# Kernel optimization log

Hardware: AMD Instinct MI355X
Metric: run time of the kernel (lower is better)

The kernel has to match this reference:

```python
import jax, jax.numpy as jnp
import numpy as np

SCORE_THRESH = 0.5
NMS_THRESH = 0.4
TOP_K = 1000  # fixed pre-NMS candidate budget (jit-safe replacement for boolean masking)
STRIDES = (8, 16, 32)
H, W = 2176, 3840


def _anchor_centers(fh, fw, stride):
    yv, xv = jnp.meshgrid(jnp.arange(fh), jnp.arange(fw), indexing='ij')
    return (jnp.stack([xv, yv], -1).reshape(-1, 2).astype(jnp.float32)) * stride  # [N,2]


def _decode_level(scores, bbox, kps, stride):
    fh, fw = H // stride, W // stride
    c = _anchor_centers(fh, fw, stride)                 # [N,2]
    s = jax.nn.sigmoid(scores.reshape(-1))              # [N]
    d = bbox.reshape(-1, 4) * stride                    # [N,4]
    boxes = jnp.concatenate([c - d[:, :2], c + d[:, 2:4]], axis=1)  # x1y1x2y2
    k = kps.reshape(-1, 5, 2) * stride + c[:, None, :]  # (x,y) pairs
    return s, boxes, k.reshape(-1, 10)


def _iou_matrix(b):
    area = (b[:, 2] - b[:, 0]) * (b[:, 3] - b[:, 1])
    lt = jnp.maximum(b[:, None, :2], b[None, :, :2])
    rb = jnp.minimum(b[:, None, 2:], b[None, :, 2:])
    wh = jnp.clip(rb - lt, 0.0)
    inter = wh[..., 0] * wh[..., 1]
    return inter / jnp.clip(area[:, None] + area[None, :] - inter, 1e-9)


def _nms_keep(iou, valid):
    n = iou.shape[0]
    ar = jnp.arange(n)

    def body(i, keep):
        sup = (iou[i] > NMS_THRESH) & (ar > i) & keep[i]
        return keep & ~sup

    return jax.lax.fori_loop(0, n, body, valid)


def reference(x, scores8, bbox8, kps8, scores16, bbox16, kps16, scores32, bbox32, kps32):
    levels = ((scores8, bbox8, kps8), (scores16, bbox16, kps16), (scores32, bbox32, kps32))
    ss, bs, ks = [], [], []
    for (s, b, k), stride in zip(levels, STRIDES):
        si, bi, ki = _decode_level(s, b, k, stride)
        ss.append(si); bs.append(bi); ks.append(ki)
    scores = jnp.concatenate(ss)   # [N_total]
    boxes = jnp.concatenate(bs)    # [N_total,4]
    kpss = jnp.concatenate(ks)     # [N_total,10]

    masked = jnp.where(scores > SCORE_THRESH, scores, -1.0)
    top_s, idx = jax.lax.top_k(masked, TOP_K)
    valid = top_s > SCORE_THRESH
    b = boxes[idx]
    k = kpss[idx]

    keep = jax.lax.stop_gradient(_nms_keep(_iou_matrix(b), valid))
    final_boxes = jnp.where(keep[:, None], b, 0.0)
    final_scores = jnp.where(keep, top_s, 0.0)
    final_kpss = jnp.where(keep[:, None], k, 0.0)
    return final_boxes, final_scores, final_kpss


def setup_inputs() -> dict:
    key = jax.random.key(0)
    ks = jax.random.split(key, 10)
    n8 = (H // 8) * (W // 8)
    n16 = (H // 16) * (W // 16)
    n32 = (H // 32) * (W // 32)
    return {
        'x': jax.random.normal(ks[0], (1, 3, H, W), jnp.float32),
        'scores8': jax.random.normal(ks[1], (1, n8, 1), jnp.float32),
        'bbox8': jax.random.uniform(ks[2], (1, n8, 4), jnp.float32),
        'kps8': jax.random.normal(ks[3], (1, n8, 10), jnp.float32),
        'scores16': jax.random.normal(ks[4], (1, n16, 1), jnp.float32),
        'bbox16': jax.random.uniform(ks[5], (1, n16, 4), jnp.float32),
        'kps16': jax.random.normal(ks[6], (1, n16, 10), jnp.float32),
        'scores32': jax.random.normal(ks[7], (1, n32, 1), jnp.float32),
        'bbox32': jax.random.uniform(ks[8], (1, n32, 4), jnp.float32),
        'kps32': jax.random.normal(ks[9], (1, n32, 10), jnp.float32),
    }
```

## Files before the change

kernel.cpp:

```cpp
#include <hip/hip_runtime.h>
#include <stdint.h>

typedef unsigned int u32;
typedef unsigned long long u64;

#define N8   130560
#define N16  32640
#define N32  8160
#define NTOT 171360
#define NTOT4 42840
#define TOPK 1000
#define NWORDS 16
#define NBINS 4096
#define BUCKET_SCALE 682.0f
#define LIST_CAP 2016
#define CPB 32
#define HIST_BLKS 168
#define RED_BLKS 32
#define RANK_BLKS 63
#define IOU_BLKS 63
#define IOU_TASKS (TOPK * NWORDS)
#define NMS_CACHE 256


#define MI_B   0
#define MI_CNT 1
#define META_U32 256

#define OFF_PART 0
#define OFF_RED  1376256
#define OFF_META 1392640
#define OFF_NZ   1393664
#define OFF_LIST 1393792
#define OFF_MASK 1409920

__device__ __forceinline__ u32 bucket_of(float x) {
  u32 b = (u32)(x * BUCKET_SCALE);
  return b > (NBINS - 1) ? (NBINS - 1) : b;
}

__device__ __forceinline__ float4 load_logit4(int v, const float* s8, const float* s16,
                                              const float* s32) {
  int e = v * 4;
  if (e < N8) return ((const float4*)s8)[v];
  if (e < N8 + N16) return ((const float4*)s16)[v - N8 / 4];
  return ((const float4*)s32)[v - (N8 + N16) / 4];
}

__device__ __forceinline__ bool iou_gt04(float4 a, float4 b) {
#pragma clang fp contract(off)
  float areaA = (a.z - a.x) * (a.w - a.y);
  float areaB = (b.z - b.x) * (b.w - b.y);
  float ltx = fmaxf(a.x, b.x);
  float lty = fmaxf(a.y, b.y);
  float rbx = fminf(a.z, b.z);
  float rby = fminf(a.w, b.w);
  float wx = rbx - ltx; wx = wx > 0.0f ? wx : 0.0f;
  float wy = rby - lty; wy = wy > 0.0f ? wy : 0.0f;
  float inter = wx * wy;
  float un = areaA + areaB - inter;
  un = un > 1e-9f ? un : 1e-9f;
  return (inter / un) > 0.4f;
}

__device__ __forceinline__ u64 valid_word(int w, u32 vcnt) {
  int lo = w * 64;
  if ((int)vcnt >= lo + 64) return ~0ull;
  if ((int)vcnt <= lo) return 0ull;
  return (1ull << (vcnt - (u32)lo)) - 1ull;
}

__global__ void __launch_bounds__(256) k1_hist(
    const float* __restrict__ s8, const float* __restrict__ s16, const float* __restrict__ s32,
    u32* __restrict__ part, u32* __restrict__ meta, u64* __restrict__ nz) {
  __shared__ u32 lh[NBINS];
  const int t = threadIdx.x, blk = blockIdx.x;
#pragma unroll
  for (int k = 0; k < 16; ++k) lh[k * 256 + t] = 0;
  __syncthreads();
  int v = blk * 256 + t;
  if (v < NTOT4) {
    float4 x = load_logit4(v, s8, s16, s32);
    if (x.x > 0.0f) atomicAdd(&lh[bucket_of(x.x)], 1u);
    if (x.y > 0.0f) atomicAdd(&lh[bucket_of(x.y)], 1u);
    if (x.z > 0.0f) atomicAdd(&lh[bucket_of(x.z)], 1u);
    if (x.w > 0.0f) atomicAdd(&lh[bucket_of(x.w)], 1u);
  }
  __syncthreads();
#pragma unroll
  for (int k = 0; k < 8; ++k) {
    int w = k * 256 + t;
    part[blk * 2048 + w] = lh[2 * w] | (lh[2 * w + 1] << 16);
  }
  if (blk == 0) {
    if (t < META_U32) meta[t] = 0;
    if (t < NWORDS) nz[t] = 0ull;
  }
}

__global__ void __launch_bounds__(256) k2_reduce(
    const u32* __restrict__ part, u32* __restrict__ red) {
  __shared__ u32 llo[256], lhi[256];
  const int t = threadIdx.x, blk = blockIdx.x;
  const int w = t & 63, pp = t >> 6;
  u32 lo = 0, hi = 0;
  for (int p = pp; p < HIST_BLKS; p += 4) {
    u32 pv = part[p * 2048 + blk * 64 + w];
    lo += pv & 0xFFFFu; hi += pv >> 16;
  }
  llo[t] = lo; lhi[t] = hi;
  __syncthreads();
  if (t < 64) {
    u32 l = llo[t] + llo[64 + t] + llo[128 + t] + llo[192 + t];
    u32 h = lhi[t] + lhi[64 + t] + lhi[128 + t] + lhi[192 + t];
    red[blk * 128 + 2 * t] = l;
    red[blk * 128 + 2 * t + 1] = h;
  }
}

__global__ void __launch_bounds__(256) k3_findb(
    const u32* __restrict__ red, u32* __restrict__ meta) {
  __shared__ u32 hloc[NBINS];
  __shared__ u32 csum[256];
  const int t = threadIdx.x;
#pragma unroll
  for (int k = 0; k < 16; ++k) hloc[k * 256 + t] = red[k * 256 + t];
  __syncthreads();
  u32 sum = 0;
  int base = t * 16;
#pragma unroll
  for (int k = 0; k < 16; ++k) sum += hloc[base + k];
  csum[t] = sum;
  __syncthreads();
  for (int off = 1; off < 256; off <<= 1) {
    u32 add = (t + off < 256) ? csum[t + off] : 0u;
    __syncthreads();
    csum[t] += add;
    __syncthreads();
  }
  u32 above = (t < 255) ? csum[t + 1] : 0u;
  if (t == 0 && csum[0] < TOPK) meta[MI_B] = 0u;
  if (csum[t] >= TOPK && above < TOPK) {
    u32 cum = above, Bv = (u32)(t * 16);
    for (int b = t * 16 + 15; b >= t * 16; --b) {
      cum += hloc[b];
      if (cum >= TOPK) { Bv = (u32)b; break; }
    }
    meta[MI_B] = Bv;
  }
}

__global__ void __launch_bounds__(256) k4_compact(
    const float* __restrict__ s8, const float* __restrict__ s16, const float* __restrict__ s32,
    u32* __restrict__ meta, u64* __restrict__ list) {
  __shared__ u32 sB, sBase;
  __shared__ u32 cnt16[16];
  const int t = threadIdx.x, blk = blockIdx.x;
  const int wave = t >> 6, lane = t & 63;
  const int v = blk * 256 + t;
  if (t == 0) sB = meta[MI_B];
  float4 x = make_float4(-1.f, -1.f, -1.f, -1.f);
  if (v < NTOT4) x = load_logit4(v, s8, s16, s32);
  __syncthreads();
  const u32 B = sB;
  float c[4] = {x.x, x.y, x.z, x.w};
  u32 win = 0;
#pragma unroll
  for (int j = 0; j < 4; ++j)
    if (c[j] > 0.0f && bucket_of(c[j]) >= B) win |= 1u << j;
  u32 wpos[4], wcnt[4];
#pragma unroll
  for (int j = 0; j < 4; ++j) {
    u64 bal = __ballot((win >> j) & 1u);
    wcnt[j] = (u32)__popcll(bal);
    wpos[j] = (u32)__popcll(bal & ((1ull << lane) - 1ull));
  }
  if (lane == 0) {
#pragma unroll
    for (int j = 0; j < 4; ++j) cnt16[wave * 4 + j] = wcnt[j];
  }
  __syncthreads();
  if (t == 0) {
    u32 tot = 0, pre[16];
#pragma unroll
    for (int k = 0; k < 16; ++k) { pre[k] = tot; tot += cnt16[k]; }
#pragma unroll
    for (int k = 0; k < 16; ++k) cnt16[k] = pre[k];
    sBase = tot ? atomicAdd(&meta[MI_CNT], tot) : 0u;
  }
  __syncthreads();
#pragma unroll
  for (int j = 0; j < 4; ++j) {
    if ((win >> j) & 1u) {
      u32 dst = sBase + cnt16[wave * 4 + j] + wpos[j];
      if (dst < LIST_CAP) {
        u32 idx = (u32)(v * 4 + j);
        list[dst] = ((u64)__float_as_uint(c[j]) << 32) | (u64)(~idx);
      }
    }
  }
}

__global__ void __launch_bounds__(256) k5_rank(
    const u32* __restrict__ meta, const u64* __restrict__ list,
    const float* __restrict__ bb8,  const float* __restrict__ kp8,
    const float* __restrict__ bb16, const float* __restrict__ kp16,
    const float* __restrict__ bb32, const float* __restrict__ kp32,
    float* __restrict__ out) {
  __shared__ __align__(16) u64 keys[LIST_CAP];
  __shared__ u32 rpart[256];
  __shared__ u32 sCnt;
  const int t = threadIdx.x, blk = blockIdx.x;
  if (t == 0) { u32 cc = meta[MI_CNT]; sCnt = cc > LIST_CAP ? LIST_CAP : cc; }
  __syncthreads();
  const u32 cnt = sCnt;
  for (int j = t; j < LIST_CAP; j += 256) keys[j] = (j < (int)cnt) ? list[j] : 0ull;
  __syncthreads();
  {
    const int ci = t & 31, sl = t >> 5;
    const int c = blk * CPB + ci;
    const int chunk = ((int)cnt + 7) >> 3;
    int lo = sl * chunk; if (lo > (int)cnt) lo = (int)cnt;
    int hi = lo + chunk; if (hi > (int)cnt) hi = (int)cnt;
    u64 my = keys[c];
    int r = 0, j = lo;
    for (; j + 4 <= hi; j += 4)
      r += (keys[j] > my) + (keys[j + 1] > my) + (keys[j + 2] > my) + (keys[j + 3] > my);
    for (; j < hi; ++j) r += (keys[j] > my);
    rpart[t] = (u32)r;
  }
  __syncthreads();
  if (t < CPB) {
    const int c = blk * CPB + t;
    if (c < (int)cnt) {
      int rank = 0;
#pragma unroll
      for (int q = 0; q < 8; ++q) rank += (int)rpart[t + 32 * q];
      if (rank < TOPK) {
        u64 my = keys[c];
        float lx = __uint_as_float((u32)(my >> 32));
        float sc = (float)(1.0 / (1.0 + exp(-(double)lx)));
        u32 idx = ~((u32)my);
        float4 box;
        float kv[10];
        int p, xq, yq;
        float st;
        const float *bb, *kp;
        if (idx < N8) {
          st = 8.f;  p = (int)idx;              xq = p % 480; yq = p / 480; bb = bb8;  kp = kp8;
        } else if (idx < N8 + N16) {
          st = 16.f; p = (int)idx - N8;         xq = p % 240; yq = p / 240; bb = bb16; kp = kp16;
        } else {
          st = 32.f; p = (int)idx - (N8 + N16); xq = p % 120; yq = p / 120; bb = bb32; kp = kp32;
        }
        float cx = (float)xq * st, cy = (float)yq * st;
        {
#pragma clang fp contract(off)
          float d0 = bb[4 * p + 0] * st;
          float d1 = bb[4 * p + 1] * st;
          float d2 = bb[4 * p + 2] * st;
          float d3 = bb[4 * p + 3] * st;
          box.x = cx - d0; box.y = cy - d1; box.z = cx + d2; box.w = cy + d3;
          for (int q = 0; q < 10; ++q)
            kv[q] = kp[10 * p + q] * st + ((q & 1) ? cy : cx);
        }
        ((float4*)out)[rank] = box;
        out[4000 + rank] = sc;
#pragma unroll
        for (int q = 0; q < 10; ++q) out[5000 + 10 * rank + q] = kv[q];
      }
    } else if (c < TOPK) {
      ((float4*)out)[c] = make_float4(0.f, 0.f, 0.f, 0.f);
      out[4000 + c] = 0.f;
#pragma unroll
      for (int q = 0; q < 10; ++q) out[5000 + 10 * c + q] = 0.f;
    }
  }
}

__global__ void __launch_bounds__(256) k6_iou(
    const float* __restrict__ out, u64* __restrict__ mask, u64* __restrict__ nz) {
  __shared__ __align__(16) float4 boxes[TOPK];
  const int t = threadIdx.x, blk = blockIdx.x;
  for (int r = t; r < TOPK; r += 256) boxes[r] = ((const float4*)out)[r];
  __syncthreads();
  int task = blk * 256 + t;
  if (task < IOU_TASKS) {
    int w = task / 1000;
    int i = task - w * 1000;
    float4 a = boxes[i];
    int bse = w * 64;
    int jend = (bse + 64) < TOPK ? (bse + 64) : TOPK;
    u64 bits = 0;
    for (int j = bse; j < jend; ++j)
      if (j > i && iou_gt04(a, boxes[j])) bits |= 1ull << (j - bse);
    mask[(u64)w * 1000 + i] = bits;
    if (bits) atomicOr(&nz[i >> 6], 1ull << (i & 63));
  }
}

__global__ void __launch_bounds__(256) k7_nms(
    const u32* __restrict__ meta, const u64* __restrict__ nzWords,
    const u64* __restrict__ mask, float* __restrict__ out) {
  __shared__ __align__(16) char smem[36864];
  __shared__ u32 sPc[16], sOff17[17];
  __shared__ u64 sRem[NWORDS];
  const int t = threadIdx.x;
  u32 cc = meta[MI_CNT];
  if (cc > LIST_CAP) cc = LIST_CAP;
  const u32 vcnt = cc < TOPK ? cc : TOPK;
  u32* rows = (u32*)smem;
  u64* cache = (u64*)(smem + 4096);
  u64 nzv = 0;
  if (t < NWORDS) {
    nzv = nzWords[t] & valid_word(t, vcnt);
    sPc[t] = (u32)__popcll(nzv);
  }
  __syncthreads();
  if (t == 0) {
    u32 o = 0;
    for (int w = 0; w < NWORDS; ++w) { sOff17[w] = o; o += sPc[w]; }
    sOff17[16] = o;
  }
  __syncthreads();
  if (t < NWORDS) {
    u64 m = nzv;
    u32 o = sOff17[t];
    while (m) { int b = __builtin_ctzll(m); m &= m - 1; rows[o++] = (u32)(t * 64 + b); }
  }
  __syncthreads();
  const int S = (int)sOff17[16];
  const int Sc = S < NMS_CACHE ? S : NMS_CACHE;
  for (int idx = t; idx < Sc * NWORDS; idx += 256) {
    int s = idx >> 4, w = idx & 15;
    cache[s * NWORDS + w] = mask[(u64)w * 1000 + rows[s]];
  }
  __syncthreads();
  if (t < 64) {
    u64 remv = 0;
    for (int s = 0; s < S; ++s) {
      u32 row = rows[s];
      int c = (int)(row >> 6), b = (int)(row & 63);
      u64 remc = __shfl(remv, c);
      if (!((remc >> b) & 1ull)) {
        u64 m = 0;
        if (t < NWORDS)
          m = (s < NMS_CACHE) ? cache[s * NWORDS + t] : mask[(u64)t * 1000 + row];
        remv |= m;
      }
    }
    if (t < NWORDS) sRem[t] = valid_word(t, vcnt) & remv;
  }
  __syncthreads();
  for (int r = t; r < TOPK; r += 256) {
    if ((sRem[r >> 6] >> (r & 63)) & 1ull) {
      ((float4*)out)[r] = make_float4(0.f, 0.f, 0.f, 0.f);
      out[4000 + r] = 0.f;
#pragma unroll
      for (int q = 0; q < 10; ++q) out[5000 + 10 * r + q] = 0.f;
    }
  }
}

extern "C" void kernel_launch(void* const* d_in, const int* in_sizes, int n_in,
                              void* d_out, int out_size, void* d_ws, size_t ws_size,
                              hipStream_t stream) {
  const float* s8   = (const float*)d_in[1];
  const float* bb8  = (const float*)d_in[2];
  const float* kp8  = (const float*)d_in[3];
  const float* s16  = (const float*)d_in[4];
  const float* bb16 = (const float*)d_in[5];
  const float* kp16 = (const float*)d_in[6];
  const float* s32  = (const float*)d_in[7];
  const float* bb32 = (const float*)d_in[8];
  const float* kp32 = (const float*)d_in[9];

  char* ws = (char*)d_ws;
  u32* part    = (u32*)(ws + OFF_PART);
  u32* red     = (u32*)(ws + OFF_RED);
  u32* meta    = (u32*)(ws + OFF_META);
  u64* nzWords = (u64*)(ws + OFF_NZ);
  u64* list    = (u64*)(ws + OFF_LIST);
  u64* mask    = (u64*)(ws + OFF_MASK);
  float* out   = (float*)d_out;

  k1_hist<<<HIST_BLKS, 256, 0, stream>>>(s8, s16, s32, part, meta, nzWords);
  k2_reduce<<<RED_BLKS, 256, 0, stream>>>(part, red);
  k3_findb<<<1, 256, 0, stream>>>(red, meta);
  k4_compact<<<HIST_BLKS, 256, 0, stream>>>(s8, s16, s32, meta, list);
  k5_rank<<<RANK_BLKS, 256, 0, stream>>>(meta, list, bb8, kp8, bb16, kp16, bb32, kp32, out);
  k6_iou<<<IOU_BLKS, 256, 0, stream>>>(out, mask, nzWords);
  k7_nms<<<1, 256, 0, stream>>>(meta, nzWords, mask, out);
}
```

Measured before the change: 178.0 us.

## Fuse threshold search into compaction and IOU with NMS via last-block pattern

Measured after the change: 170.6 us. -4.1%, faster.

```diff
diff --git a/kernel.cpp b/kernel.cpp
--- a/kernel.cpp
+++ b/kernel.cpp
@@ -15,24 +15,37 @@
 #define BUCKET_SCALE 682.0f
 #define LIST_CAP 2016
 #define CPB 32
-#define HIST_BLKS 168
+#define HIST_BLKS 84
+#define HIST_THR 512
 #define RED_BLKS 32
+#define CMP_BLKS 168
 #define RANK_BLKS 63
 #define IOU_BLKS 63
 #define IOU_TASKS (TOPK * NWORDS)
 #define NMS_CACHE 256
-
-
-#define MI_B   0
-#define MI_CNT 1
+#define POISON 0xAAAAAAAAu
+
+
+#define MI_CNT 0
+#define MI_IOU 128
 #define META_U32 256
 
 #define OFF_PART 0
-#define OFF_RED  1376256
-#define OFF_META 1392640
-#define OFF_NZ   1393664
-#define OFF_LIST 1393792
-#define OFF_MASK 1409920
+#define OFF_RED  688128
+#define OFF_META 704512
+#define OFF_NZ   705536
+#define OFF_LIST 705664
+#define OFF_MASK 721792
+
+__device__ __forceinline__ u32 ald32(const u32* p) {
+  return __hip_atomic_load(p, __ATOMIC_RELAXED, __HIP_MEMORY_SCOPE_AGENT);
+}
+__device__ __forceinline__ u64 ald64(const u64* p) {
+  return __hip_atomic_load(p, __ATOMIC_RELAXED, __HIP_MEMORY_SCOPE_AGENT);
+}
+__device__ __forceinline__ void ast64(u64* p, u64 v) {
+  __hip_atomic_store(p, v, __ATOMIC_RELAXED, __HIP_MEMORY_SCOPE_AGENT);
+}
 
 __device__ __forceinline__ u32 bucket_of(float x) {
   u32 b = (u32)(x * BUCKET_SCALE);
@@ -70,15 +83,15 @@
   return (1ull << (vcnt - (u32)lo)) - 1ull;
 }
 
-__global__ void __launch_bounds__(256) k1_hist(
+__global__ void __launch_bounds__(HIST_THR) k1_hist(
     const float* __restrict__ s8, const float* __restrict__ s16, const float* __restrict__ s32,
     u32* __restrict__ part, u32* __restrict__ meta, u64* __restrict__ nz) {
   __shared__ u32 lh[NBINS];
   const int t = threadIdx.x, blk = blockIdx.x;
 #pragma unroll
-  for (int k = 0; k < 16; ++k) lh[k * 256 + t] = 0;
-  __syncthreads();
-  int v = blk * 256 + t;
+  for (int k = 0; k < 8; ++k) lh[k * HIST_THR + t] = 0;
+  __syncthreads();
+  int v = blk * HIST_THR + t;
   if (v < NTOT4) {
     float4 x = load_logit4(v, s8, s16, s32);
     if (x.x > 0.0f) atomicAdd(&lh[bucket_of(x.x)], 1u);
@@ -88,8 +101,8 @@
   }
   __syncthreads();
 #pragma unroll
-  for (int k = 0; k < 8; ++k) {
-    int w = k * 256 + t;
+  for (int k = 0; k < 4; ++k) {
+    int w = k * HIST_THR + t;
     part[blk * 2048 + w] = lh[2 * w] | (lh[2 * w + 1] << 16);
   }
   if (blk == 0) {
@@ -118,11 +131,18 @@
   }
 }
 
-__global__ void __launch_bounds__(256) k3_findb(
-    const u32* __restrict__ red, u32* __restrict__ meta) {
+__global__ void __launch_bounds__(256) k4_compact(
+    const float* __restrict__ s8, const float* __restrict__ s16, const float* __restrict__ s32,
+    const u32* __restrict__ red, u32* __restrict__ meta, u64* __restrict__ list) {
   __shared__ u32 hloc[NBINS];
   __shared__ u32 csum[256];
-  const int t = threadIdx.x;
+  __shared__ u32 sB, sBase;
+  __shared__ u32 cnt16[16];
+  const int t = threadIdx.x, blk = blockIdx.x;
+  const int wave = t >> 6, lane = t & 63;
+  const int v = blk * 256 + t;
+  float4 x = make_float4(-1.f, -1.f, -1.f, -1.f);
+  if (v < NTOT4) x = load_logit4(v, s8, s16, s32);
 #pragma unroll
   for (int k = 0; k < 16; ++k) hloc[k * 256 + t] = red[k * 256 + t];
   __syncthreads();
@@ -139,28 +159,15 @@
     __syncthreads();
   }
   u32 above = (t < 255) ? csum[t + 1] : 0u;
-  if (t == 0 && csum[0] < TOPK) meta[MI_B] = 0u;
+  if (t == 0 && csum[0] < TOPK) sB = 0u;
   if (csum[t] >= TOPK && above < TOPK) {
     u32 cum = above, Bv = (u32)(t * 16);
     for (int b = t * 16 + 15; b >= t * 16; --b) {
       cum += hloc[b];
       if (cum >= TOPK) { Bv = (u32)b; break; }
     }
-    meta[MI_B] = Bv;
-  }
-}
-
-__global__ void __launch_bounds__(256) k4_compact(
-    const float* __restrict__ s8, const float* __restrict__ s16, const float* __restrict__ s32,
-    u32* __restrict__ meta, u64* __restrict__ list) {
-  __shared__ u32 sB, sBase;
-  __shared__ u32 cnt16[16];
-  const int t = threadIdx.x, blk = blockIdx.x;
-  const int wave = t >> 6, lane = t & 63;
-  const int v = blk * 256 + t;
-  if (t == 0) sB = meta[MI_B];
-  float4 x = make_float4(-1.f, -1.f, -1.f, -1.f);
-  if (v < NTOT4) x = load_logit4(v, s8, s16, s32);
+    sB = Bv;
+  }
   __syncthreads();
   const u32 B = sB;
   float c[4] = {x.x, x.y, x.z, x.w};
@@ -278,10 +285,15 @@
   }
 }
 
-__global__ void __launch_bounds__(256) k6_iou(
-    const float* __restrict__ out, u64* __restrict__ mask, u64* __restrict__ nz) {
-  __shared__ __align__(16) float4 boxes[TOPK];
+__global__ void __launch_bounds__(256) k67_iou_nms(
+    u32* meta, u64* nzWords, u64* mask, float* out) {
+  __shared__ __align__(16) char smem[36864];
+  __shared__ int isLast;
+  __shared__ u32 sPc[16], sOff17[17];
+  __shared__ u64 sRem[NWORDS];
   const int t = threadIdx.x, blk = blockIdx.x;
+
+  float4* boxes = (float4*)smem;
   for (int r = t; r < TOPK; r += 256) boxes[r] = ((const float4*)out)[r];
   __syncthreads();
   int task = blk * 256 + t;
@@ -294,18 +306,16 @@
     u64 bits = 0;
     for (int j = bse; j < jend; ++j)
       if (j > i && iou_gt04(a, boxes[j])) bits |= 1ull << (j - bse);
-    mask[(u64)w * 1000 + i] = bits;
-    if (bits) atomicOr(&nz[i >> 6], 1ull << (i & 63));
-  }
-}
-
-__global__ void __launch_bounds__(256) k7_nms(
-    const u32* __restrict__ meta, const u64* __restrict__ nzWords,
-    const u64* __restrict__ mask, float* __restrict__ out) {
-  __shared__ __align__(16) char smem[36864];
-  __shared__ u32 sPc[16], sOff17[17];
-  __shared__ u64 sRem[NWORDS];
-  const int t = threadIdx.x;
+    ast64(&mask[(u64)w * 1000 + i], bits);
+    if (bits) atomicOr(&nzWords[i >> 6], 1ull << (i & 63));
+  }
+  __syncthreads();
+  if (t == 0)
+    isLast = (__hip_atomic_fetch_add(&meta[MI_IOU], 1u, __ATOMIC_RELAXED,
+                                     __HIP_MEMORY_SCOPE_AGENT) == (u32)(IOU_BLKS - 1));
+  __syncthreads();
+  if (!isLast) return;
+
   u32 cc = meta[MI_CNT];
   if (cc > LIST_CAP) cc = LIST_CAP;
   const u32 vcnt = cc < TOPK ? cc : TOPK;
@@ -313,7 +323,7 @@
   u64* cache = (u64*)(smem + 4096);
   u64 nzv = 0;
   if (t < NWORDS) {
-    nzv = nzWords[t] & valid_word(t, vcnt);
+    nzv = ald64(&nzWords[t]) & valid_word(t, vcnt);
     sPc[t] = (u32)__popcll(nzv);
   }
   __syncthreads();
@@ -333,7 +343,7 @@
   const int Sc = S < NMS_CACHE ? S : NMS_CACHE;
   for (int idx = t; idx < Sc * NWORDS; idx += 256) {
     int s = idx >> 4, w = idx & 15;
-    cache[s * NWORDS + w] = mask[(u64)w * 1000 + rows[s]];
+    cache[s * NWORDS + w] = ald64(&mask[(u64)w * 1000 + rows[s]]);
   }
   __syncthreads();
   if (t < 64) {
@@ -345,7 +355,7 @@
       if (!((remc >> b) & 1ull)) {
         u64 m = 0;
         if (t < NWORDS)
-          m = (s < NMS_CACHE) ? cache[s * NWORDS + t] : mask[(u64)t * 1000 + row];
+          m = (s < NMS_CACHE) ? cache[s * NWORDS + t] : ald64(&mask[(u64)t * 1000 + row]);
         remv |= m;
       }
     }
@@ -384,11 +394,9 @@
   u64* mask    = (u64*)(ws + OFF_MASK);
   float* out   = (float*)d_out;
 
-  k1_hist<<<HIST_BLKS, 256, 0, stream>>>(s8, s16, s32, part, meta, nzWords);
+  k1_hist<<<HIST_BLKS, HIST_THR, 0, stream>>>(s8, s16, s32, part, meta, nzWords);
   k2_reduce<<<RED_BLKS, 256, 0, stream>>>(part, red);
-  k3_findb<<<1, 256, 0, stream>>>(red, meta);
-  k4_compact<<<HIST_BLKS, 256, 0, stream>>>(s8, s16, s32, meta, list);
+  k4_compact<<<CMP_BLKS, 256, 0, stream>>>(s8, s16, s32, red, meta, list);
   k5_rank<<<RANK_BLKS, 256, 0, stream>>>(meta, list, bb8, kp8, bb16, kp16, bb32, kp32, out);
-  k6_iou<<<IOU_BLKS, 256, 0, stream>>>(out, mask, nzWords);
-  k7_nms<<<1, 256, 0, stream>>>(meta, nzWords, mask, out);
-}
+  k67_iou_nms<<<IOU_BLKS, 256, 0, stream>>>(meta, nzWords, mask, out);
+}
```
